# Kernel optimization log

Measured on AMD Instinct MI355X. Metric: run time of the kernel, lower is better.

The kernel has to match this reference:

```python
import jax, jax.numpy as jnp
import numpy as np

B, S, P, E, H, NCTX = 4, 1024, 1024, 1024, 16, 2048
D = E // H


def setup_inputs() -> dict:
    key = jax.random.key(0)
    k0, k1, k2, k3 = jax.random.split(key, 4)
    x = jax.random.normal(k0, (B, S, E), jnp.float32)
    layer_past = jax.random.normal(k1, (2, B, H, P, D), jnp.float32)
    w_attn = jax.random.normal(k2, (E, 3 * E), jnp.float32) * 0.02
    b_attn = jnp.zeros((3 * E,), jnp.float32)
    w_proj = jax.random.normal(k3, (E, E), jnp.float32) * 0.02
    b_proj = jnp.zeros((E,), jnp.float32)
    return {"x": x, "layer_past": layer_past, "w_attn": w_attn,
            "b_attn": b_attn, "w_proj": w_proj, "b_proj": b_proj}


def reference(x, layer_past, w_attn, b_attn, w_proj, b_proj):
    # c_attn: Conv1D == linear with weight [nx, nf]
    qkv = x @ w_attn + b_attn                       # [B,S,3E]
    q, k, v = jnp.split(qkv, 3, axis=-1)

    def heads(t):                                   # [B,S,E] -> [B,H,S,D]
        return t.reshape(B, -1, H, D).transpose(0, 2, 1, 3)

    q, k, v = heads(q), heads(k), heads(v)
    # KV-cache concat: layer_past[0] is [B,H,P,D] (module transposes to
    # [B,H,D,P] then concats on last dim; equivalent to concat on seq dim).
    k = jnp.concatenate([layer_past[0], k], axis=2)  # [B,H,ns,D]
    v = jnp.concatenate([layer_past[1], v], axis=2)  # [B,H,ns,D]
    present = jnp.stack([k, v])                      # [2,B,H,ns,D]

    nd, ns = q.shape[2], k.shape[2]
    w = jnp.einsum('bhqd,bhkd->bhqk', q, k) / jnp.sqrt(jnp.float32(D))
    mask = jnp.tril(jnp.ones((NCTX, NCTX), jnp.float32))[ns - nd:ns, :ns]
    w = w * mask - 10000.0 * (1.0 - mask)
    a = jnp.einsum('bhqk,bhkd->bhqd', jax.nn.softmax(w, axis=-1), v)
    a = a.transpose(0, 2, 1, 3).reshape(B, -1, E)    # merge heads
    out = a @ w_proj + b_proj
    return out, present
```

## Files before the change

kernel.cpp:

```cpp
#include <hip/hip_runtime.h>
#include <hip/hip_bf16.h>

#define BB 4
#define SS 1024
#define PP 1024
#define EE 1024
#define HH 16
#define DD 64
#define NS 2048
#define E3 3072
#define VOFF 8388608
#define VPAST 4194304

typedef __attribute__((ext_vector_type(8))) short short8;
typedef __attribute__((ext_vector_type(4))) float floatx4;
typedef __attribute__((ext_vector_type(16))) float floatx16;
typedef __attribute__((ext_vector_type(4))) unsigned uintx4;

__device__ __forceinline__ short f2bf(float f) {
    return (short)(__bfloat16_as_ushort(__float2bfloat16(f)));
}

__device__ __forceinline__ unsigned cvtpk(float lo, float hi) {
    unsigned r;
    asm("v_cvt_pk_bf16_f32 %0, %1, %2" : "=v"(r) : "v"(lo), "v"(hi));
    return r;
}

__device__ __forceinline__ void plswap(unsigned &a, unsigned &b) {
    asm("v_permlane32_swap_b32 %0, %1" : "+v"(a), "+v"(b));
}

__device__ __forceinline__ void gload16(const void* g, void* l) {
    __builtin_amdgcn_global_load_lds(
        (const __attribute__((address_space(1))) void*)g,
        (__attribute__((address_space(3))) void*)l, 16, 0, 0);
}

__global__ __launch_bounds__(256) void cvt_copy_k(
    const float* __restrict__ x, const float* __restrict__ past,
    short* __restrict__ xb, short* __restrict__ kbp, short* __restrict__ vbp,
    float* __restrict__ present)
{
    size_t e0 = ((size_t)blockIdx.x * 256 + threadIdx.x) * 8;
    if (e0 < 4194304) {
        float4 a0 = *(const float4*)(x + e0);
        float4 a1 = *(const float4*)(x + e0 + 4);
        short8 s;
        s[0] = f2bf(a0.x); s[1] = f2bf(a0.y); s[2] = f2bf(a0.z); s[3] = f2bf(a0.w);
        s[4] = f2bf(a1.x); s[5] = f2bf(a1.y); s[6] = f2bf(a1.z); s[7] = f2bf(a1.w);
        *(short8*)(xb + e0) = s;
    } else {
        size_t r = e0 - 4194304;
        int sec = (r >= 4194304);
        if (sec) r -= 4194304;
        const float* src = past + (sec ? VPAST : 0) + r;
        int row = (int)(r >> 6);
        int bh = row >> 10, t = row & 1023, d = (int)(r & 63);
        size_t off = ((size_t)bh * NS + t) * DD + d;
        float4 a0 = *(const float4*)src;
        float4 a1 = *(const float4*)(src + 4);
        short8 s;
        s[0] = f2bf(a0.x); s[1] = f2bf(a0.y); s[2] = f2bf(a0.z); s[3] = f2bf(a0.w);
        s[4] = f2bf(a1.x); s[5] = f2bf(a1.y); s[6] = f2bf(a1.z); s[7] = f2bf(a1.w);
        *(short8*)((sec ? vbp : kbp) + off) = s;
        float* pd = present + (sec ? VOFF : 0) + off;
        *(float4*)(pd)     = a0;
        *(float4*)(pd + 4) = a1;
    }
}

__global__ __launch_bounds__(256) void wtrans_k(
    const float* __restrict__ wa, const float* __restrict__ wp,
    short* __restrict__ wab, short* __restrict__ wpb)
{
    __shared__ short Ts[64][72];
    int bid = blockIdx.x;
    const float* src; short* dst; int n0, k0, Nsrc;
    if (bid < 768) { k0 = (bid & 15) * 64; n0 = (bid >> 4) * 64; src = wa; dst = wab; Nsrc = E3; }
    else { bid -= 768; k0 = (bid & 15) * 64; n0 = (bid >> 4) * 64; src = wp; dst = wpb; Nsrc = EE; }
    int tid = threadIdx.x;
    int r = tid >> 2, c = (tid & 3) * 16;
    const float* s = src + (size_t)(k0 + r) * Nsrc + n0 + c;
    float4 a0 = *(const float4*)(s);
    float4 a1 = *(const float4*)(s + 4);
    float4 a2 = *(const float4*)(s + 8);
    float4 a3 = *(const float4*)(s + 12);
    Ts[c +  0][r] = f2bf(a0.x); Ts[c +  1][r] = f2bf(a0.y);
    Ts[c +  2][r] = f2bf(a0.z); Ts[c +  3][r] = f2bf(a0.w);
    Ts[c +  4][r] = f2bf(a1.x); Ts[c +  5][r] = f2bf(a1.y);
    Ts[c +  6][r] = f2bf(a1.z); Ts[c +  7][r] = f2bf(a1.w);
    Ts[c +  8][r] = f2bf(a2.x); Ts[c +  9][r] = f2bf(a2.y);
    Ts[c + 10][r] = f2bf(a2.z); Ts[c + 11][r] = f2bf(a2.w);
    Ts[c + 12][r] = f2bf(a3.x); Ts[c + 13][r] = f2bf(a3.y);
    Ts[c + 14][r] = f2bf(a3.z); Ts[c + 15][r] = f2bf(a3.w);
    __syncthreads();
    int n = tid >> 2, kc = (tid & 3) * 16;
    short8 v0 = *(const short8*)&Ts[n][kc];
    short8 v1 = *(const short8*)&Ts[n][kc + 8];
    short* d = dst + (size_t)(n0 + n) * EE + k0 + kc;
    *(short8*)d = v0;
    *(short8*)(d + 8) = v1;
}

template<int MODE, int NT>
__global__ __launch_bounds__(256) void gemm_bt_k(
    const short* __restrict__ A,
    const short* __restrict__ Bt,
    const float* __restrict__ bias,
    float* __restrict__ outf,
    short* __restrict__ qb, short* __restrict__ kbp, short* __restrict__ vbp,
    float* __restrict__ present,
    int N)
{
    constexpr int MR = (NT == 128) ? 4 : 2;
    __shared__ __align__(16) short As[2][128 * 32];
    __shared__ __align__(16) short Bs[2][NT * 32];
    int tid = threadIdx.x;
    int wave = tid >> 6, lane = tid & 63;
    int fr = lane & 15, quad = lane >> 4;
    int wm = (NT == 128) ? (wave >> 1) : wave;
    int wn = (NT == 128) ? (wave & 1) : 0;
    int hw = blockIdx.y * gridDim.x + blockIdx.x;
    int nwg = gridDim.x * gridDim.y;
    int work = (hw & 7) * (nwg >> 3) + (hw >> 3);
    int bx = work / gridDim.y, by = work - bx * gridDim.y;
    int m0 = bx * 128, n0 = by * NT;

    floatx4 acc[MR][4];
#pragma unroll
    for (int m = 0; m < MR; ++m)
#pragma unroll
        for (int n = 0; n < 4; ++n) acc[m][n] = (floatx4){0.f, 0.f, 0.f, 0.f};

    auto STAGE = [&](int k0, int buf) {
#pragma unroll
        for (int p = 0; p < 2; ++p) {
            int idx = p * 256 + tid;
            int row = idx >> 2, ch = idx & 3;
            gload16(A + (size_t)(m0 + row) * 1024 + k0 + ch * 8,
                    &As[buf][(p * 256 + wave * 64) * 8]);
        }
#pragma unroll
        for (int p = 0; p < NT / 64; ++p) {
            int idx = p * 256 + tid;
            int row = idx >> 2, ch = idx & 3;
            gload16(Bt + (size_t)(n0 + row) * 1024 + k0 + ch * 8,
                    &Bs[buf][(p * 256 + wave * 64) * 8]);
        }
    };

    STAGE(0, 0);
    __syncthreads();
    for (int k0 = 0; k0 < 1024; k0 += 32) {
        int cur = (k0 >> 5) & 1;
        if (k0 + 32 < 1024) STAGE(k0 + 32, cur ^ 1);
        short8 af[MR], bf[4];
#pragma unroll
        for (int m = 0; m < MR; ++m)
            af[m] = *(const short8*)(&As[cur][(wm * (MR * 16) + m * 16 + fr) * 32 + quad * 8]);
#pragma unroll
        for (int n = 0; n < 4; ++n)
            bf[n] = *(const short8*)(&Bs[cur][(wn * 64 + n * 16 + fr) * 32 + quad * 8]);
#pragma unroll
        for (int m = 0; m < MR; ++m)
#pragma unroll
            for (int n = 0; n < 4; ++n)
                acc[m][n] = __builtin_amdgcn_mfma_f32_16x16x32_bf16(af[m], bf[n], acc[m][n], 0, 0, 0);
        __syncthreads();
    }
#pragma unroll
    for (int n = 0; n < 4; ++n) {
        int gc = n0 + wn * 64 + n * 16 + fr;
        float bv = bias[gc];
#pragma unroll
        for (int m = 0; m < MR; ++m) {
#pragma unroll
            for (int r = 0; r < 4; ++r) {
                int gr = m0 + wm * (MR * 16) + m * 16 + quad * 4 + r;
                float val = acc[m][n][r] + bv;
                if (MODE == 1) {
                    outf[(size_t)gr * N + gc] = val;
                } else {
                    int sec = gc >> 10, h = (gc >> 6) & 15, d = gc & 63;
                    int b = gr >> 10, sq = gr & 1023;
                    size_t bh = (size_t)(b * HH + h);
                    if (sec == 0) {
                        qb[(bh * SS + sq) * DD + d] = f2bf(val * 0.18033688f);
                    } else {
                        size_t off = (bh * NS + PP + sq) * DD + d;
                        if (sec == 1) { present[off] = val;        kbp[off] = f2bf(val); }
                        else          { present[VOFF + off] = val; vbp[off] = f2bf(val); }
                    }
                }
            }
        }
    }
}

__global__ __launch_bounds__(512) void flash_attn_k(
    const short* __restrict__ qb, const short* __restrict__ kbp,
    const short* __restrict__ vbp, short* __restrict__ ab)
{
    __shared__ __align__(16) short smem[16384];
    short* Ks = smem;
    short* Vs = smem + 8192;

    int tid = threadIdx.x;
    int wave = tid >> 6, lane = tid & 63;
    int qcol = lane & 31, hi = lane >> 5;
    int qg = wave >> 1, kh = wave & 1;

    int bid = blockIdx.x;
    int work = (bid & 7) * 64 + (bid >> 3);
    int bh = work >> 3;
    int q0 = (work & 7) * 128;

    const short* qrow = qb + ((size_t)bh * SS + q0 + qg * 32 + qcol) * DD + hi * 8;
    short8 qf[4];
#pragma unroll
    for (int i = 0; i < 4; ++i) qf[i] = *(const short8*)(qrow + i * 16);

    const short* kbase = kbp + (size_t)bh * NS * DD;
    const short* vbase = vbp + (size_t)bh * NS * DD;

    float m_r = -1e30f, l_r = 0.f;
    floatx16 Oa[2];
#pragma unroll
    for (int dt = 0; dt < 2; ++dt)
#pragma unroll
        for (int r = 0; r < 16; ++r) Oa[dt][r] = 0.f;

    int vkey = tid & 63, vd0 = (tid >> 6) * 8;
    int qminw = PP + q0 + qg * 32;
    int qmaxw = qminw + 31;

    short8 vs0;
    auto KISSUE = [&](int cc, int bufi) {
        const short* kc = kbase + (size_t)cc * 64 * DD;
        int row = tid >> 3, ch = tid & 7;
        gload16(kc + row * 64 + ((ch ^ (row & 7)) * 8),
                Ks + bufi * 4096 + wave * 512);
    };
    auto VLOAD = [&](int cc) {
        vs0 = *(const short8*)(vbase + ((size_t)cc * 64 + vkey) * DD + vd0);
    };
    auto VWRITE = [&](int bufi) {
        short* Vd = Vs + bufi * 4096;
#pragma unroll
        for (int i = 0; i < 8; ++i) {
            int di = vd0 + i;
            Vd[di * 64 + (((vkey >> 3) ^ (di & 7)) << 3) + (vkey & 7)] = vs0[i];
        }
    };

    int nchunks = 18 + (q0 >> 6);
    KISSUE(0, 0); VLOAD(0); VWRITE(0);
    __syncthreads();

    for (int c = 0; c < nchunks; ++c) {
        int t0 = c * 64;
        int cur = c & 1;
        if (c + 1 < nchunks) { KISSUE(c + 1, cur ^ 1); VLOAD(c + 1); }
        if (t0 <= qmaxw) {
            const short* Kc = Ks + cur * 4096;
            const short* Vc = Vs + cur * 4096;
            floatx16 Sa;
#pragma unroll
            for (int r = 0; r < 16; ++r) Sa[r] = 0.f;
            int key = kh * 32 + qcol;
            int rbase = key * 64, rx = key & 7;
#pragma unroll
            for (int d0 = 0; d0 < 4; ++d0) {
                short8 kf = *(const short8*)(Kc + rbase + (((d0 * 2 + hi) ^ rx) * 8));
                Sa = __builtin_amdgcn_mfma_f32_32x32x16_bf16(kf, qf[d0], Sa, 0, 0, 0);
            }
            if (t0 + 63 > qminw) {
                int qa = qminw + qcol;
#pragma unroll
                for (int r = 0; r < 16; ++r) {
                    int ka = t0 + kh * 32 + (r & 3) + 8 * (r >> 2) + 4 * hi;
                    if (ka > qa) Sa[r] = -1e30f;
                }
            }
            float mx0 = fmaxf(Sa[0], Sa[1]),  mx1 = fmaxf(Sa[2], Sa[3]);
            float mx2 = fmaxf(Sa[4], Sa[5]),  mx3 = fmaxf(Sa[6], Sa[7]);
            mx0 = fmaxf(mx0, fmaxf(Sa[8], Sa[9]));
            mx1 = fmaxf(mx1, fmaxf(Sa[10], Sa[11]));
            mx2 = fmaxf(mx2, fmaxf(Sa[12], Sa[13]));
            mx3 = fmaxf(mx3, fmaxf(Sa[14], Sa[15]));
            float mx = fmaxf(fmaxf(mx0, mx1), fmaxf(mx2, mx3));
            mx = fmaxf(mx, __shfl_xor(mx, 32, 64));
            if (!__all(mx <= m_r + 11.5416f)) {
                float mnew = fmaxf(m_r, mx);
                float al = exp2f(m_r - mnew);
                l_r *= al;
#pragma unroll
                for (int dt = 0; dt < 2; ++dt)
#pragma unroll
                    for (int r = 0; r < 16; ++r) Oa[dt][r] *= al;
                m_r = mnew;
            }
            float s0 = 0.f, s1 = 0.f, s2 = 0.f, s3 = 0.f;
#pragma unroll
            for (int r = 0; r < 16; r += 4) {
                float p0 = exp2f(Sa[r]     - m_r);
                float p1 = exp2f(Sa[r + 1] - m_r);
                float p2 = exp2f(Sa[r + 2] - m_r);
                float p3 = exp2f(Sa[r + 3] - m_r);
                Sa[r] = p0; Sa[r + 1] = p1; Sa[r + 2] = p2; Sa[r + 3] = p3;
                s0 += p0; s1 += p1; s2 += p2; s3 += p3;
            }
            float sum = (s0 + s1) + (s2 + s3);
            sum += __shfl_xor(sum, 32, 64);
            l_r += sum;
            short8 pfr[2];
            {
                unsigned w0 = cvtpk(Sa[0],  Sa[1]);
                unsigned w2 = cvtpk(Sa[4],  Sa[5]);
                unsigned w1 = cvtpk(Sa[2],  Sa[3]);
                unsigned w3 = cvtpk(Sa[6],  Sa[7]);
                plswap(w0, w2);
                plswap(w1, w3);
                union { uintx4 u; short8 s; } cv0;
                cv0.u = (uintx4){w0, w1, w2, w3};
                pfr[0] = cv0.s;
                unsigned x0 = cvtpk(Sa[8],  Sa[9]);
                unsigned x2 = cvtpk(Sa[12], Sa[13]);
                unsigned x1 = cvtpk(Sa[10], Sa[11]);
                unsigned x3 = cvtpk(Sa[14], Sa[15]);
                plswap(x0, x2);
                plswap(x1, x3);
                union { uintx4 u; short8 s; } cv1;
                cv1.u = (uintx4){x0, x1, x2, x3};
                pfr[1] = cv1.s;
            }
#pragma unroll
            for (int ks = 0; ks < 2; ++ks) {
                int chunkb = kh * 4 + ks * 2 + hi;
#pragma unroll
                for (int dt = 0; dt < 2; ++dt) {
                    int row = dt * 32 + qcol;
                    short8 vf = *(const short8*)(Vc + row * 64 + ((chunkb ^ (row & 7)) << 3));
                    Oa[dt] = __builtin_amdgcn_mfma_f32_32x32x16_bf16(vf, pfr[ks], Oa[dt], 0, 0, 0);
                }
            }
        }
        if (c + 1 < nchunks) VWRITE(cur ^ 1);
        __syncthreads();
    }

    float* mlf = (float*)smem;
    if (hi == 0) {
        mlf[(wave * 32 + qcol) * 2]     = m_r;
        mlf[(wave * 32 + qcol) * 2 + 1] = l_r;
    }
    __syncthreads();
    float m_o = mlf[((wave ^ 1) * 32 + qcol) * 2];
    float l_o = mlf[((wave ^ 1) * 32 + qcol) * 2 + 1];
    __syncthreads();
    float M = fmaxf(m_r, m_o);
    float sc = exp2f(m_r - M);
    float l_tot = l_r * sc + l_o * exp2f(m_o - M);
    float* Of = (float*)smem;
    if (kh == 0) {
#pragma unroll
        for (int dt = 0; dt < 2; ++dt)
#pragma unroll
            for (int r = 0; r < 16; ++r) {
                int d = dt * 32 + (r & 3) + 8 * (r >> 2) + 4 * hi;
                Of[(qg * 64 + d) * 32 + qcol] = Oa[dt][r] * sc;
            }
    }
    __syncthreads();
    if (kh == 1) {
        float inv = 1.f / l_tot;
#pragma unroll
        for (int dt = 0; dt < 2; ++dt)
#pragma unroll
            for (int r = 0; r < 16; ++r) {
                int d = dt * 32 + (r & 3) + 8 * (r >> 2) + 4 * hi;
                Oa[dt][r] = (Of[(qg * 64 + d) * 32 + qcol] + Oa[dt][r] * sc) * inv;
            }
    }
    __syncthreads();
    short* Ot = smem;
    if (kh == 1) {
#pragma unroll
        for (int dt = 0; dt < 2; ++dt)
#pragma unroll
            for (int r = 0; r < 16; ++r) {
                int d = dt * 32 + (r & 3) + 8 * (r >> 2) + 4 * hi;
                Ot[(qg * 32 + qcol) * 72 + d] = f2bf(Oa[dt][r]);
            }
    }
    __syncthreads();
    int r2 = tid >> 2;
    int qgi = r2 >> 5, qi = r2 & 31, doff = (tid & 3) * 16;
    int b = bh >> 4, h = bh & 15;
    int qa = q0 + qgi * 32 + qi;
    short* dst = ab + ((size_t)(b * SS + qa)) * EE + h * DD + doff;
    const short* srcr = Ot + (qgi * 32 + qi) * 72 + doff;
    *(short8*)(dst)     = *(const short8*)(srcr);
    *(short8*)(dst + 8) = *(const short8*)(srcr + 8);
}

extern "C" void kernel_launch(void* const* d_in, const int* in_sizes, int n_in,
                              void* d_out, int out_size, void* d_ws, size_t ws_size,
                              hipStream_t stream) {
    const float* x      = (const float*)d_in[0];
    const float* past   = (const float*)d_in[1];
    const float* w_attn = (const float*)d_in[2];
    const float* b_attn = (const float*)d_in[3];
    const float* w_proj = (const float*)d_in[4];
    const float* b_proj = (const float*)d_in[5];
    float* out = (float*)d_out;
    float* present = out + (size_t)BB * SS * EE;

    short* ws  = (short*)d_ws;
    short* xb  = ws;
    short* wab = xb  + 4194304;
    short* wpb = wab + 3145728;
    short* qb  = wpb + 1048576;
    short* kbp = qb  + 4194304;
    short* vbp = kbp + 8388608;
    short* ab  = vbp + 8388608;

    cvt_copy_k<<<6144, 256, 0, stream>>>(x, past, xb, kbp, vbp, present);
    wtrans_k<<<1024, 256, 0, stream>>>(w_attn, w_proj, wab, wpb);
    gemm_bt_k<0, 128><<<dim3(32, 24), 256, 0, stream>>>(xb, wab, b_attn, nullptr,
                                                        qb, kbp, vbp, present, E3);
    flash_attn_k<<<512, 512, 0, stream>>>(qb, kbp, vbp, ab);
    gemm_bt_k<1, 64><<<dim3(32, 16), 256, 0, stream>>>(ab, wpb, b_proj, out,
                                                       nullptr, nullptr, nullptr, nullptr, EE);
}
```

Measured before the change: 297.5 us.

## Store V transposed and load K/V fragments directly from global in attention

V (both the cached past and the newly projected part) is now written in a d-major transposed bf16 layout, produced by the weight-transpose kernel and by the QKV GEMM epilogue. This lets the flash attention kernel read MFMA operand fragments for K and V straight from global memory, with no LDS staging. Each wave pair now splits 32-key chunks between its two waves instead of sharing a 64-key LDS tile, which removes the per-chunk __syncthreads and LDS swizzle writes. The trade-off is uncoalesced, strided global reads in the inner loop, with no software prefetch and more reliance on cache hits. The GEMM epilogue's V writes also become scattered with an NS stride.

New measurement: 334.8 us. +12.5%, slower.

```diff
diff --git a/kernel.cpp b/kernel.cpp
--- a/kernel.cpp
+++ b/kernel.cpp
@@ -39,7 +39,7 @@
 
 __global__ __launch_bounds__(256) void cvt_copy_k(
     const float* __restrict__ x, const float* __restrict__ past,
-    short* __restrict__ xb, short* __restrict__ kbp, short* __restrict__ vbp,
+    short* __restrict__ xb, short* __restrict__ kbp,
     float* __restrict__ present)
 {
     size_t e0 = ((size_t)blockIdx.x * 256 + threadIdx.x) * 8;
@@ -60,10 +60,12 @@
         size_t off = ((size_t)bh * NS + t) * DD + d;
         float4 a0 = *(const float4*)src;
         float4 a1 = *(const float4*)(src + 4);
-        short8 s;
-        s[0] = f2bf(a0.x); s[1] = f2bf(a0.y); s[2] = f2bf(a0.z); s[3] = f2bf(a0.w);
-        s[4] = f2bf(a1.x); s[5] = f2bf(a1.y); s[6] = f2bf(a1.z); s[7] = f2bf(a1.w);
-        *(short8*)((sec ? vbp : kbp) + off) = s;
+        if (!sec) {
+            short8 s;
+            s[0] = f2bf(a0.x); s[1] = f2bf(a0.y); s[2] = f2bf(a0.z); s[3] = f2bf(a0.w);
+            s[4] = f2bf(a1.x); s[5] = f2bf(a1.y); s[6] = f2bf(a1.z); s[7] = f2bf(a1.w);
+            *(short8*)(kbp + off) = s;
+        }
         float* pd = present + (sec ? VOFF : 0) + off;
         *(float4*)(pd)     = a0;
         *(float4*)(pd + 4) = a1;
@@ -72,16 +74,30 @@
 
 __global__ __launch_bounds__(256) void wtrans_k(
     const float* __restrict__ wa, const float* __restrict__ wp,
-    short* __restrict__ wab, short* __restrict__ wpb)
+    const float* __restrict__ past,
+    short* __restrict__ wab, short* __restrict__ wpb, short* __restrict__ vtb)
 {
     __shared__ short Ts[64][72];
     int bid = blockIdx.x;
-    const float* src; short* dst; int n0, k0, Nsrc;
-    if (bid < 768) { k0 = (bid & 15) * 64; n0 = (bid >> 4) * 64; src = wa; dst = wab; Nsrc = E3; }
-    else { bid -= 768; k0 = (bid & 15) * 64; n0 = (bid >> 4) * 64; src = wp; dst = wpb; Nsrc = EE; }
+    const float* s0; short* d0p; int RS, DS2;
+    if (bid < 768) {
+        int k0 = (bid & 15) * 64, n0 = (bid >> 4) * 64;
+        s0 = wa + (size_t)k0 * E3 + n0; RS = E3;
+        d0p = wab + (size_t)n0 * EE + k0; DS2 = EE;
+    } else if (bid < 1024) {
+        int b2 = bid - 768;
+        int k0 = (b2 & 15) * 64, n0 = (b2 >> 4) * 64;
+        s0 = wp + (size_t)k0 * EE + n0; RS = EE;
+        d0p = wpb + (size_t)n0 * EE + k0; DS2 = EE;
+    } else {
+        int b2 = bid - 1024;
+        int bh = b2 >> 4, t0 = (b2 & 15) * 64;
+        s0 = past + VPAST + ((size_t)bh * PP + t0) * 64; RS = 64;
+        d0p = vtb + (size_t)bh * 64 * NS + t0; DS2 = NS;
+    }
     int tid = threadIdx.x;
     int r = tid >> 2, c = (tid & 3) * 16;
-    const float* s = src + (size_t)(k0 + r) * Nsrc + n0 + c;
+    const float* s = s0 + (size_t)r * RS + c;
     float4 a0 = *(const float4*)(s);
     float4 a1 = *(const float4*)(s + 4);
     float4 a2 = *(const float4*)(s + 8);
@@ -98,7 +114,7 @@
     int n = tid >> 2, kc = (tid & 3) * 16;
     short8 v0 = *(const short8*)&Ts[n][kc];
     short8 v1 = *(const short8*)&Ts[n][kc + 8];
-    short* d = dst + (size_t)(n0 + n) * EE + k0 + kc;
+    short* d = d0p + (size_t)n * DS2 + kc;
     *(short8*)d = v0;
     *(short8*)(d + 8) = v1;
 }
@@ -109,7 +125,7 @@
     const short* __restrict__ Bt,
     const float* __restrict__ bias,
     float* __restrict__ outf,
-    short* __restrict__ qb, short* __restrict__ kbp, short* __restrict__ vbp,
+    short* __restrict__ qb, short* __restrict__ kbp, short* __restrict__ vtb,
     float* __restrict__ present,
     int N)
 {
@@ -189,8 +205,13 @@
                         qb[(bh * SS + sq) * DD + d] = f2bf(val * 0.18033688f);
                     } else {
                         size_t off = (bh * NS + PP + sq) * DD + d;
-                        if (sec == 1) { present[off] = val;        kbp[off] = f2bf(val); }
-                        else          { present[VOFF + off] = val; vbp[off] = f2bf(val); }
+                        if (sec == 1) {
+                            present[off] = val;
+                            kbp[off] = f2bf(val);
+                        } else {
+                            present[VOFF + off] = val;
+                            vtb[(bh * 64 + d) * NS + PP + sq] = f2bf(val);
+                        }
                     }
                 }
             }
@@ -200,29 +221,28 @@
 
 __global__ __launch_bounds__(512) void flash_attn_k(
     const short* __restrict__ qb, const short* __restrict__ kbp,
-    const short* __restrict__ vbp, short* __restrict__ ab)
+    const short* __restrict__ vtb, short* __restrict__ ab)
 {
     __shared__ __align__(16) short smem[16384];
-    short* Ks = smem;
-    short* Vs = smem + 8192;
 
     int tid = threadIdx.x;
     int wave = tid >> 6, lane = tid & 63;
     int qcol = lane & 31, hi = lane >> 5;
-    int qg = wave >> 1, kh = wave & 1;
+    int qt = wave >> 1, sp = wave & 1;
 
     int bid = blockIdx.x;
     int work = (bid & 7) * 64 + (bid >> 3);
     int bh = work >> 3;
-    int q0 = (work & 7) * 128;
-
-    const short* qrow = qb + ((size_t)bh * SS + q0 + qg * 32 + qcol) * DD + hi * 8;
+    int qb0 = (work & 7) * 128;
+    int q32 = qb0 + qt * 32;
+
+    const short* qrow = qb + ((size_t)bh * SS + q32 + qcol) * DD + hi * 8;
     short8 qf[4];
 #pragma unroll
     for (int i = 0; i < 4; ++i) qf[i] = *(const short8*)(qrow + i * 16);
 
     const short* kbase = kbp + (size_t)bh * NS * DD;
-    const short* vbase = vbp + (size_t)bh * NS * DD;
+    const short* vbase = vtb + (size_t)bh * 64 * NS;
 
     float m_r = -1e30f, l_r = 0.f;
     floatx16 Oa[2];
@@ -231,123 +251,91 @@
 #pragma unroll
         for (int r = 0; r < 16; ++r) Oa[dt][r] = 0.f;
 
-    int vkey = tid & 63, vd0 = (tid >> 6) * 8;
-    int qminw = PP + q0 + qg * 32;
-    int qmaxw = qminw + 31;
-
-    short8 vs0;
-    auto KISSUE = [&](int cc, int bufi) {
-        const short* kc = kbase + (size_t)cc * 64 * DD;
-        int row = tid >> 3, ch = tid & 7;
-        gload16(kc + row * 64 + ((ch ^ (row & 7)) * 8),
-                Ks + bufi * 4096 + wave * 512);
-    };
-    auto VLOAD = [&](int cc) {
-        vs0 = *(const short8*)(vbase + ((size_t)cc * 64 + vkey) * DD + vd0);
-    };
-    auto VWRITE = [&](int bufi) {
-        short* Vd = Vs + bufi * 4096;
-#pragma unroll
-        for (int i = 0; i < 8; ++i) {
-            int di = vd0 + i;
-            Vd[di * 64 + (((vkey >> 3) ^ (di & 7)) << 3) + (vkey & 7)] = vs0[i];
-        }
-    };
-
-    int nchunks = 18 + (q0 >> 6);
-    KISSUE(0, 0); VLOAD(0); VWRITE(0);
-    __syncthreads();
-
-    for (int c = 0; c < nchunks; ++c) {
-        int t0 = c * 64;
-        int cur = c & 1;
-        if (c + 1 < nchunks) { KISSUE(c + 1, cur ^ 1); VLOAD(c + 1); }
-        if (t0 <= qmaxw) {
-            const short* Kc = Ks + cur * 4096;
-            const short* Vc = Vs + cur * 4096;
-            floatx16 Sa;
-#pragma unroll
-            for (int r = 0; r < 16; ++r) Sa[r] = 0.f;
-            int key = kh * 32 + qcol;
-            int rbase = key * 64, rx = key & 7;
-#pragma unroll
-            for (int d0 = 0; d0 < 4; ++d0) {
-                short8 kf = *(const short8*)(Kc + rbase + (((d0 * 2 + hi) ^ rx) * 8));
-                Sa = __builtin_amdgcn_mfma_f32_32x32x16_bf16(kf, qf[d0], Sa, 0, 0, 0);
+    int cmax = 33 + (q32 >> 5);
+    for (int c = sp; c < cmax; c += 2) {
+        int t0 = c << 5;
+        const short* kc = kbase + (size_t)(t0 + qcol) * DD + hi * 8;
+        short8 kf0 = *(const short8*)(kc);
+        short8 kf1 = *(const short8*)(kc + 16);
+        short8 kf2 = *(const short8*)(kc + 32);
+        short8 kf3 = *(const short8*)(kc + 48);
+        const short* vc0 = vbase + (size_t)qcol * NS + t0 + hi * 8;
+        const short* vc1 = vbase + (size_t)(32 + qcol) * NS + t0 + hi * 8;
+        short8 vf00 = *(const short8*)(vc0);
+        short8 vf01 = *(const short8*)(vc0 + 16);
+        short8 vf10 = *(const short8*)(vc1);
+        short8 vf11 = *(const short8*)(vc1 + 16);
+        floatx16 Sa;
+#pragma unroll
+        for (int r = 0; r < 16; ++r) Sa[r] = 0.f;
+        Sa = __builtin_amdgcn_mfma_f32_32x32x16_bf16(kf0, qf[0], Sa, 0, 0, 0);
+        Sa = __builtin_amdgcn_mfma_f32_32x32x16_bf16(kf1, qf[1], Sa, 0, 0, 0);
+        Sa = __builtin_amdgcn_mfma_f32_32x32x16_bf16(kf2, qf[2], Sa, 0, 0, 0);
+        Sa = __builtin_amdgcn_mfma_f32_32x32x16_bf16(kf3, qf[3], Sa, 0, 0, 0);
+        if (t0 + 31 > PP + q32) {
+            int qa = PP + q32 + qcol;
+#pragma unroll
+            for (int r = 0; r < 16; ++r) {
+                int ka = t0 + (r & 3) + 8 * (r >> 2) + 4 * hi;
+                if (ka > qa) Sa[r] = -1e30f;
             }
-            if (t0 + 63 > qminw) {
-                int qa = qminw + qcol;
-#pragma unroll
-                for (int r = 0; r < 16; ++r) {
-                    int ka = t0 + kh * 32 + (r & 3) + 8 * (r >> 2) + 4 * hi;
-                    if (ka > qa) Sa[r] = -1e30f;
-                }
-            }
-            float mx0 = fmaxf(Sa[0], Sa[1]),  mx1 = fmaxf(Sa[2], Sa[3]);
-            float mx2 = fmaxf(Sa[4], Sa[5]),  mx3 = fmaxf(Sa[6], Sa[7]);
-            mx0 = fmaxf(mx0, fmaxf(Sa[8], Sa[9]));
-            mx1 = fmaxf(mx1, fmaxf(Sa[10], Sa[11]));
-            mx2 = fmaxf(mx2, fmaxf(Sa[12], Sa[13]));
-            mx3 = fmaxf(mx3, fmaxf(Sa[14], Sa[15]));
-            float mx = fmaxf(fmaxf(mx0, mx1), fmaxf(mx2, mx3));
-            mx = fmaxf(mx, __shfl_xor(mx, 32, 64));
-            if (!__all(mx <= m_r + 11.5416f)) {
-                float mnew = fmaxf(m_r, mx);
-                float al = exp2f(m_r - mnew);
-                l_r *= al;
-#pragma unroll
-                for (int dt = 0; dt < 2; ++dt)
-#pragma unroll
-                    for (int r = 0; r < 16; ++r) Oa[dt][r] *= al;
-                m_r = mnew;
-            }
-            float s0 = 0.f, s1 = 0.f, s2 = 0.f, s3 = 0.f;
-#pragma unroll
-            for (int r = 0; r < 16; r += 4) {
-                float p0 = exp2f(Sa[r]     - m_r);
-                float p1 = exp2f(Sa[r + 1] - m_r);
-                float p2 = exp2f(Sa[r + 2] - m_r);
-                float p3 = exp2f(Sa[r + 3] - m_r);
-                Sa[r] = p0; Sa[r + 1] = p1; Sa[r + 2] = p2; Sa[r + 3] = p3;
-                s0 += p0; s1 += p1; s2 += p2; s3 += p3;
-            }
-            float sum = (s0 + s1) + (s2 + s3);
-            sum += __shfl_xor(sum, 32, 64);
-            l_r += sum;
-            short8 pfr[2];
-            {
-                unsigned w0 = cvtpk(Sa[0],  Sa[1]);
-                unsigned w2 = cvtpk(Sa[4],  Sa[5]);
-                unsigned w1 = cvtpk(Sa[2],  Sa[3]);
-                unsigned w3 = cvtpk(Sa[6],  Sa[7]);
-                plswap(w0, w2);
-                plswap(w1, w3);
-                union { uintx4 u; short8 s; } cv0;
-                cv0.u = (uintx4){w0, w1, w2, w3};
-                pfr[0] = cv0.s;
-                unsigned x0 = cvtpk(Sa[8],  Sa[9]);
-                unsigned x2 = cvtpk(Sa[12], Sa[13]);
-                unsigned x1 = cvtpk(Sa[10], Sa[11]);
-                unsigned x3 = cvtpk(Sa[14], Sa[15]);
-                plswap(x0, x2);
-                plswap(x1, x3);
-                union { uintx4 u; short8 s; } cv1;
-                cv1.u = (uintx4){x0, x1, x2, x3};
-                pfr[1] = cv1.s;
-            }
-#pragma unroll
-            for (int ks = 0; ks < 2; ++ks) {
-                int chunkb = kh * 4 + ks * 2 + hi;
-#pragma unroll
-                for (int dt = 0; dt < 2; ++dt) {
-                    int row = dt * 32 + qcol;
-                    short8 vf = *(const short8*)(Vc + row * 64 + ((chunkb ^ (row & 7)) << 3));
-                    Oa[dt] = __builtin_amdgcn_mfma_f32_32x32x16_bf16(vf, pfr[ks], Oa[dt], 0, 0, 0);
-                }
-            }
-        }
-        if (c + 1 < nchunks) VWRITE(cur ^ 1);
-        __syncthreads();
+        }
+        float mx0 = fmaxf(Sa[0], Sa[1]),  mx1 = fmaxf(Sa[2], Sa[3]);
+        float mx2 = fmaxf(Sa[4], Sa[5]),  mx3 = fmaxf(Sa[6], Sa[7]);
+        mx0 = fmaxf(mx0, fmaxf(Sa[8], Sa[9]));
+        mx1 = fmaxf(mx1, fmaxf(Sa[10], Sa[11]));
+        mx2 = fmaxf(mx2, fmaxf(Sa[12], Sa[13]));
+        mx3 = fmaxf(mx3, fmaxf(Sa[14], Sa[15]));
+        float mx = fmaxf(fmaxf(mx0, mx1), fmaxf(mx2, mx3));
+        mx = fmaxf(mx, __shfl_xor(mx, 32, 64));
+        if (!__all(mx <= m_r + 11.5416f)) {
+            float mnew = fmaxf(m_r, mx);
+            float al = exp2f(m_r - mnew);
+            l_r *= al;
+#pragma unroll
+            for (int dt = 0; dt < 2; ++dt)
+#pragma unroll
+                for (int r = 0; r < 16; ++r) Oa[dt][r] *= al;
+            m_r = mnew;
+        }
+        float s0 = 0.f, s1 = 0.f, s2 = 0.f, s3 = 0.f;
+#pragma unroll
+        for (int r = 0; r < 16; r += 4) {
+            float p0 = exp2f(Sa[r]     - m_r);
+            float p1 = exp2f(Sa[r + 1] - m_r);
+            float p2 = exp2f(Sa[r + 2] - m_r);
+            float p3 = exp2f(Sa[r + 3] - m_r);
+            Sa[r] = p0; Sa[r + 1] = p1; Sa[r + 2] = p2; Sa[r + 3] = p3;
+            s0 += p0; s1 += p1; s2 += p2; s3 += p3;
+        }
+        float sum = (s0 + s1) + (s2 + s3);
+        sum += __shfl_xor(sum, 32, 64);
+        l_r += sum;
+        short8 pfr[2];
+        {
+            unsigned w0 = cvtpk(Sa[0],  Sa[1]);
+            unsigned w2 = cvtpk(Sa[4],  Sa[5]);
+            unsigned w1 = cvtpk(Sa[2],  Sa[3]);
+            unsigned w3 = cvtpk(Sa[6],  Sa[7]);
+            plswap(w0, w2);
+            plswap(w1, w3);
+            union { uintx4 u; short8 s; } cv0;
+            cv0.u = (uintx4){w0, w1, w2, w3};
+            pfr[0] = cv0.s;
+            unsigned x0 = cvtpk(Sa[8],  Sa[9]);
+            unsigned x2 = cvtpk(Sa[12], Sa[13]);
+            unsigned x1 = cvtpk(Sa[10], Sa[11]);
+            unsigned x3 = cvtpk(Sa[14], Sa[15]);
+            plswap(x0, x2);
+            plswap(x1, x3);
+            union { uintx4 u; short8 s; } cv1;
+            cv1.u = (uintx4){x0, x1, x2, x3};
+            pfr[1] = cv1.s;
+        }
+        Oa[0] = __builtin_amdgcn_mfma_f32_32x32x16_bf16(vf00, pfr[0], Oa[0], 0, 0, 0);
+        Oa[0] = __builtin_amdgcn_mfma_f32_32x32x16_bf16(vf01, pfr[1], Oa[0], 0, 0, 0);
+        Oa[1] = __builtin_amdgcn_mfma_f32_32x32x16_bf16(vf10, pfr[0], Oa[1], 0, 0, 0);
+        Oa[1] = __builtin_amdgcn_mfma_f32_32x32x16_bf16(vf11, pfr[1], Oa[1], 0, 0, 0);
     }
 
     float* mlf = (float*)smem;
@@ -363,42 +351,42 @@
     float sc = exp2f(m_r - M);
     float l_tot = l_r * sc + l_o * exp2f(m_o - M);
     float* Of = (float*)smem;
-    if (kh == 0) {
+    if (sp == 0) {
 #pragma unroll
         for (int dt = 0; dt < 2; ++dt)
 #pragma unroll
             for (int r = 0; r < 16; ++r) {
                 int d = dt * 32 + (r & 3) + 8 * (r >> 2) + 4 * hi;
-                Of[(qg * 64 + d) * 32 + qcol] = Oa[dt][r] * sc;
+                Of[(qt * 64 + d) * 32 + qcol] = Oa[dt][r] * sc;
             }
     }
     __syncthreads();
-    if (kh == 1) {
+    if (sp == 1) {
         float inv = 1.f / l_tot;
 #pragma unroll
         for (int dt = 0; dt < 2; ++dt)
 #pragma unroll
             for (int r = 0; r < 16; ++r) {
                 int d = dt * 32 + (r & 3) + 8 * (r >> 2) + 4 * hi;
-                Oa[dt][r] = (Of[(qg * 64 + d) * 32 + qcol] + Oa[dt][r] * sc) * inv;
+                Oa[dt][r] = (Of[(qt * 64 + d) * 32 + qcol] + Oa[dt][r] * sc) * inv;
             }
     }
     __syncthreads();
     short* Ot = smem;
-    if (kh == 1) {
+    if (sp == 1) {
 #pragma unroll
         for (int dt = 0; dt < 2; ++dt)
 #pragma unroll
             for (int r = 0; r < 16; ++r) {
                 int d = dt * 32 + (r & 3) + 8 * (r >> 2) + 4 * hi;
-                Ot[(qg * 32 + qcol) * 72 + d] = f2bf(Oa[dt][r]);
+                Ot[(qt * 32 + qcol) * 72 + d] = f2bf(Oa[dt][r]);
             }
     }
     __syncthreads();
     int r2 = tid >> 2;
     int qgi = r2 >> 5, qi = r2 & 31, doff = (tid & 3) * 16;
     int b = bh >> 4, h = bh & 15;
-    int qa = q0 + qgi * 32 + qi;
+    int qa = qb0 + qgi * 32 + qi;
     short* dst = ab + ((size_t)(b * SS + qa)) * EE + h * DD + doff;
     const short* srcr = Ot + (qgi * 32 + qi) * 72 + doff;
     *(short8*)(dst)     = *(const short8*)(srcr);
@@ -423,14 +411,14 @@
     short* wpb = wab + 3145728;
     short* qb  = wpb + 1048576;
     short* kbp = qb  + 4194304;
-    short* vbp = kbp + 8388608;
-    short* ab  = vbp + 8388608;
-
-    cvt_copy_k<<<6144, 256, 0, stream>>>(x, past, xb, kbp, vbp, present);
-    wtrans_k<<<1024, 256, 0, stream>>>(w_attn, w_proj, wab, wpb);
+    short* vtb = kbp + 8388608;
+    short* ab  = vtb + 8388608;
+
+    cvt_copy_k<<<6144, 256, 0, stream>>>(x, past, xb, kbp, present);
+    wtrans_k<<<2048, 256, 0, stream>>>(w_attn, w_proj, past, wab, wpb, vtb);
     gemm_bt_k<0, 128><<<dim3(32, 24), 256, 0, stream>>>(xb, wab, b_attn, nullptr,
-                                                        qb, kbp, vbp, present, E3);
-    flash_attn_k<<<512, 512, 0, stream>>>(qb, kbp, vbp, ab);
+                                                        qb, kbp, vtb, present, E3);
+    flash_attn_k<<<512, 512, 0, stream>>>(qb, kbp, vtb, ab);
     gemm_bt_k<1, 64><<<dim3(32, 16), 256, 0, stream>>>(ab, wpb, b_proj, out,
                                                        nullptr, nullptr, nullptr, nullptr, EE);
 }
```
